# Kernel tuning notes

Measured on AMD Instinct MI355X. Metric: run time of the kernel, lower is better.

## Reference

```python
import jax, jax.numpy as jnp
import numpy as np

D = 384      # d_model
H = 6        # num_heads
K = 8        # k_neighbors
B = 8        # batch
N = 2048     # num points
EPS = 1e-5


def _layer_norm(x, g, b):
    m = jnp.mean(x, axis=-1, keepdims=True)
    v = jnp.var(x, axis=-1, keepdims=True)
    return (x - m) * jax.lax.rsqrt(v + EPS) * g + b


def setup_inputs() -> dict:
    key = jax.random.key(0)
    ks = jax.random.split(key, 12)
    s = 0.02
    return {
        "coords": jax.random.normal(ks[0], (B, 3, N), jnp.float32),
        "features": jax.random.normal(ks[1], (B, D, N), jnp.float32),
        "ln1_g": jnp.ones((D,), jnp.float32),
        "ln1_b": jnp.zeros((D,), jnp.float32),
        "w_qkv": jax.random.normal(ks[2], (D, 3 * D), jnp.float32) * s,
        "w_attn_out": jax.random.normal(ks[3], (D, D), jnp.float32) * s,
        "b_attn_out": jnp.zeros((D,), jnp.float32),
        "ga_wq": jax.random.normal(ks[4], (D, D), jnp.float32) * s,
        "ga_wk": jax.random.normal(ks[5], (D, D), jnp.float32) * s,
        "ga_wv": jax.random.normal(ks[6], (D, D), jnp.float32) * s,
        "merge_w": jax.random.normal(ks[7], (2 * D, D), jnp.float32) * s,
        "merge_b": jnp.zeros((D,), jnp.float32),
        "ln2_g": jnp.ones((D,), jnp.float32),
        "ln2_b": jnp.zeros((D,), jnp.float32),
        "ff_w1": jax.random.normal(ks[8], (D, 2 * D), jnp.float32) * s,
        "ff_b1": jnp.zeros((2 * D,), jnp.float32),
        "ff_w2": jax.random.normal(ks[9], (2 * D, D), jnp.float32) * s,
        "ff_b2": jnp.zeros((D,), jnp.float32),
    }


def reference(coords, features, ln1_g, ln1_b, w_qkv, w_attn_out, b_attn_out,
              ga_wq, ga_wk, ga_wv, merge_w, merge_b, ln2_g, ln2_b,
              ff_w1, ff_b1, ff_w2, ff_b2):
    b, d, n = features.shape
    dh = d // H
    f = jnp.swapaxes(features, 1, 2)          # [B, N, D]
    nf = _layer_norm(f, ln1_g, ln1_b)         # [B, N, D]

    # --- dense multi-head self-attention branch ---
    qkv = nf @ w_qkv                           # [B, N, 3D]
    q, k, v = jnp.split(qkv, 3, axis=-1)
    def heads(x):
        return x.reshape(b, n, H, dh).transpose(0, 2, 1, 3)  # [B, H, N, dh]
    scores = jnp.einsum('bhqd,bhkd->bhqk', heads(q), heads(k)) / jnp.sqrt(jnp.float32(dh))
    attn = jnp.einsum('bhqk,bhkd->bhqd', jax.nn.softmax(scores, axis=-1), heads(v))
    attn = attn.transpose(0, 2, 1, 3).reshape(b, n, d)
    attn = attn @ w_attn_out + b_attn_out      # output projection

    # --- KNN graph-attention branch over normalized features ---
    c = jnp.swapaxes(coords, 1, 2)             # [B, N, 3]
    sq = jnp.sum(c * c, axis=-1)               # [B, N]
    d2 = sq[:, :, None] + sq[:, None, :] - 2.0 * jnp.einsum('bnd,bmd->bnm', c, c)
    _, idx = jax.lax.top_k(-d2, K)             # [B, N, K] nearest-neighbor indices
    nbrs = jax.vmap(lambda fe, i: fe[i])(nf, idx)  # [B, N, K, D]
    gq = nf @ ga_wq                             # [B, N, D]
    gk = nbrs @ ga_wk                           # [B, N, K, D]
    gv = nbrs @ ga_wv
    gs = jnp.einsum('bnd,bnkd->bnk', gq, gk) / jnp.sqrt(jnp.float32(d))
    geom = jnp.einsum('bnk,bnkd->bnd', jax.nn.softmax(gs, axis=-1), gv)  # [B, N, D]

    # --- merge + residual + FFN ---
    merged = jnp.concatenate([attn, geom], axis=-1) @ merge_w + merge_b
    f = f + merged
    h = _layer_norm(f, ln2_g, ln2_b)
    f = f + (jax.nn.gelu(h @ ff_w1 + ff_b1) @ ff_w2 + ff_b2)
    return jnp.swapaxes(f, 1, 2)               # [B, D, N]
```

## Files before the change

### kernel.cpp

```cpp
#include <hip/hip_runtime.h>
#include <hip/hip_bf16.h>
#include <cstdint>

#define D_MODEL 384
#define NHEAD 6
#define DHEAD 64
#define NPTS 2048
#define BATCH 8

typedef __attribute__((ext_vector_type(8))) short short8;
typedef __attribute__((ext_vector_type(4))) short short4v;
typedef __attribute__((ext_vector_type(4))) float floatx4;
typedef __attribute__((ext_vector_type(2))) unsigned int u32x2;

__device__ __forceinline__ float bf2f(unsigned short u) {
    return __uint_as_float(((unsigned int)u) << 16);
}

__device__ __forceinline__ unsigned short f2bf(float f) {
    unsigned int u = __float_as_uint(f);
    unsigned int r = (u + 0x7FFFu + ((u >> 16) & 1u)) >> 16;
    return (unsigned short)r;
}

__device__ __forceinline__ unsigned cvtpk(float lo, float hi) {
    unsigned r;
    asm("v_cvt_pk_bf16_f32 %0, %1, %2" : "=v"(r) : "v"(lo), "v"(hi));
    return r;
}

__device__ __forceinline__ floatx4 mfma16(short4v a, short4v b, floatx4 c) {
#if __has_builtin(__builtin_amdgcn_mfma_f32_16x16x16bf16_1k)
    return __builtin_amdgcn_mfma_f32_16x16x16bf16_1k(a, b, c, 0, 0, 0);
#else
    floatx4 d;
    asm("v_mfma_f32_16x16x16_bf16 %0, %1, %2, %3" : "=v"(d) : "v"(a), "v"(b), "v"(c));
    return d;
#endif
}

__device__ __forceinline__ float gelu_tanh(float x) {
    float x3 = x * x * x;
    return 0.5f * x * (1.0f + tanhf(0.7978845608028654f * (x + 0.044715f * x3)));
}

__device__ __forceinline__ void gload_lds16(const unsigned short* g, unsigned short* l) {
    __builtin_amdgcn_global_load_lds(
        (const __attribute__((address_space(1))) unsigned int*)g,
        (__attribute__((address_space(3))) unsigned int*)l, 16, 0, 0);
}

__global__ __launch_bounds__(256) void k_wprep(
    const float* __restrict__ wqkv, const float* __restrict__ wao,
    const float* __restrict__ wq, const float* __restrict__ wk,
    const float* __restrict__ wv, const float* __restrict__ wm,
    const float* __restrict__ w1, const float* __restrict__ w2,
    unsigned short* __restrict__ qkvT, unsigned short* __restrict__ aoT,
    unsigned short* __restrict__ gaT, unsigned short* __restrict__ mT,
    unsigned short* __restrict__ f1T, unsigned short* __restrict__ f2T) {
    __shared__ float tile[32][33];
    int id = blockIdx.x;
    const float* src;
    unsigned short* dst;
    int K, N;
    if (id < 432)       {            src = wqkv; dst = qkvT;            K = 384; N = 1152; }
    else if (id < 576)  { id -= 432; src = wao;  dst = aoT;             K = 384; N = 384; }
    else if (id < 720)  { id -= 576; src = wq;   dst = gaT;             K = 384; N = 384; }
    else if (id < 864)  { id -= 720; src = wk;   dst = gaT + 384 * 384; K = 384; N = 384; }
    else if (id < 1008) { id -= 864; src = wv;   dst = gaT + 768 * 384; K = 384; N = 384; }
    else if (id < 1296) { id -= 1008; src = wm;  dst = mT;              K = 768; N = 384; }
    else if (id < 1584) { id -= 1296; src = w1;  dst = f1T;             K = 384; N = 768; }
    else                { id -= 1584; src = w2;  dst = f2T;             K = 768; N = 384; }
    int ntiles = N >> 5;
    int nt = id % ntiles, kt = id / ntiles;
    int tx = threadIdx.x, ty = threadIdx.y;
#pragma unroll
    for (int i = 0; i < 32; i += 8)
        tile[ty + i][tx] = src[(size_t)(kt * 32 + ty + i) * N + nt * 32 + tx];
    __syncthreads();
#pragma unroll
    for (int i = 0; i < 32; i += 8)
        dst[(size_t)(nt * 32 + ty + i) * K + kt * 32 + tx] = f2bf(tile[tx][ty + i]);
}

__global__ __launch_bounds__(256) void k_transpose_in(const float* __restrict__ feat,
                                                      unsigned short* __restrict__ f) {
    __shared__ float tile[32][33];
    int b = blockIdx.z;
    int n0 = blockIdx.x * 32, d0 = blockIdx.y * 32;
    int tx = threadIdx.x, ty = threadIdx.y;
#pragma unroll
    for (int i = 0; i < 32; i += 8)
        tile[ty + i][tx] = feat[((size_t)b * D_MODEL + d0 + ty + i) * NPTS + n0 + tx];
    __syncthreads();
#pragma unroll
    for (int i = 0; i < 32; i += 8)
        f[((size_t)b * NPTS + n0 + ty + i) * D_MODEL + d0 + tx] = f2bf(tile[tx][ty + i]);
}

__global__ __launch_bounds__(256) void k_transpose_out(const unsigned short* __restrict__ f,
                                                       float* __restrict__ out) {
    __shared__ float tile[32][33];
    int b = blockIdx.z;
    int d0 = blockIdx.x * 32, n0 = blockIdx.y * 32;
    int tx = threadIdx.x, ty = threadIdx.y;
#pragma unroll
    for (int i = 0; i < 32; i += 8)
        tile[ty + i][tx] = bf2f(f[((size_t)b * NPTS + n0 + ty + i) * D_MODEL + d0 + tx]);
    __syncthreads();
#pragma unroll
    for (int i = 0; i < 32; i += 8)
        out[((size_t)b * D_MODEL + d0 + ty + i) * NPTS + n0 + tx] = tile[tx][ty + i];
}

__global__ __launch_bounds__(256) void k_vt(const unsigned short* __restrict__ qkv,
                                            unsigned short* __restrict__ vt) {
    __shared__ unsigned short tile[32][33];
    int b = blockIdx.z;
    int h = blockIdx.y >> 1, d0 = (blockIdx.y & 1) * 32;
    int n0 = blockIdx.x * 32;
    int tx = threadIdx.x, ty = threadIdx.y;
#pragma unroll
    for (int i = 0; i < 32; i += 8)
        tile[ty + i][tx] =
            qkv[((size_t)b * NPTS + n0 + ty + i) * 1152 + 768 + h * 64 + d0 + tx];
    __syncthreads();
#pragma unroll
    for (int i = 0; i < 32; i += 8)
        vt[(((size_t)(b * NHEAD + h) * 64) + d0 + ty + i) * NPTS + n0 + tx] = tile[tx][ty + i];
}

__global__ __launch_bounds__(128) void k_layernorm(const unsigned short* __restrict__ x,
                                                   const float* __restrict__ g,
                                                   const float* __restrict__ bt,
                                                   unsigned short* __restrict__ y) {
    int row = blockIdx.x, t = threadIdx.x;
    const unsigned short* xr = x + (size_t)row * D_MODEL;
    float v0 = bf2f(xr[t]), v1 = bf2f(xr[t + 128]), v2 = bf2f(xr[t + 256]);
    float s = v0 + v1 + v2;
    float s2 = v0 * v0 + v1 * v1 + v2 * v2;
#pragma unroll
    for (int off = 32; off > 0; off >>= 1) {
        s += __shfl_xor(s, off, 64);
        s2 += __shfl_xor(s2, off, 64);
    }
    __shared__ float ps[2], ps2[2];
    if ((t & 63) == 0) { ps[t >> 6] = s; ps2[t >> 6] = s2; }
    __syncthreads();
    s = ps[0] + ps[1];
    s2 = ps2[0] + ps2[1];
    float mean = s * (1.0f / 384.0f);
    float var = s2 * (1.0f / 384.0f) - mean * mean;
    var = fmaxf(var, 0.0f);
    float inv = 1.0f / sqrtf(var + 1e-5f);
    unsigned short* yr = y + (size_t)row * D_MODEL;
    yr[t]       = f2bf((v0 - mean) * inv * g[t]       + bt[t]);
    yr[t + 128] = f2bf((v1 - mean) * inv * g[t + 128] + bt[t + 128]);
    yr[t + 256] = f2bf((v2 - mean) * inv * g[t + 256] + bt[t + 256]);
}

__global__ __launch_bounds__(256) void k_knn(const float* __restrict__ coords,
                                             int* __restrict__ idx) {
    __shared__ float4 cpts[NPTS];
    int b = blockIdx.x >> 9;
    int q0 = (blockIdx.x & 511) * 4;
    const float* cb = coords + (size_t)b * 3 * NPTS;
    int tid = threadIdx.x;
#pragma unroll
    for (int i = 0; i < 8; i++) {
        int m = tid + i * 256;
        float x = cb[m], y = cb[NPTS + m], z = cb[2 * NPTS + m];
        float sq = __fadd_rn(__fadd_rn(__fmul_rn(x, x), __fmul_rn(y, y)), __fmul_rn(z, z));
        cpts[m] = make_float4(x, y, z, sq);
    }
    __syncthreads();
    int wv = tid >> 6, lane = tid & 63;
    int n = q0 + wv;
    float4 qp = cpts[n];
    float qx = qp.x, qy = qp.y, qz = qp.z, sqn = qp.w;
    unsigned keys[32];
    unsigned h[8];
#pragma unroll
    for (int k = 0; k < 8; k++) h[k] = 0xFFFFFFFFu;
#pragma unroll
    for (int j = 0; j < 32; j++) {
        float4 cp = cpts[j * 64 + lane];
        float dot = __fadd_rn(__fadd_rn(__fmul_rn(qx, cp.x), __fmul_rn(qy, cp.y)),
                              __fmul_rn(qz, cp.z));
        float d2 = __fsub_rn(__fadd_rn(sqn, cp.w), __fmul_rn(2.0f, dot));
        unsigned u = __float_as_uint(d2);
        u ^= (unsigned)(((int)u >> 31)) | 0x80000000u;
        keys[j] = u;
        unsigned cur = u;
#pragma unroll
        for (int t2 = 0; t2 < 8; t2++) {
            unsigned lo = h[t2] < cur ? h[t2] : cur;
            cur = h[t2] < cur ? cur : h[t2];
            h[t2] = lo;
        }
    }
    unsigned curh = h[0];
    unsigned T8 = 0;
#pragma unroll
    for (int r = 0; r < 8; r++) {
        unsigned w = curh;
#pragma unroll
        for (int off = 1; off < 64; off <<= 1) {
            unsigned o = __shfl_xor(w, off, 64);
            w = o < w ? o : w;
        }
        T8 = w;
        if (r < 7) {
            unsigned long long mask = __ballot(curh == w);
            if (curh == w && (mask & ((1ull << lane) - 1ull)) == 0) {
#pragma unroll
                for (int t2 = 0; t2 < 7; t2++) h[t2] = h[t2 + 1];
                h[7] = 0xFFFFFFFFu;
                curh = h[0];
            }
        }
    }
    int* outr = idx + ((size_t)b * NPTS + n) * 8;
    int cnt = 0;
    unsigned meq = 0xFFFFFFFFu;
#pragma unroll
    for (int j = 0; j < 32; j++) {
        unsigned m = (unsigned)(j * 64 + lane);
        bool strict = keys[j] < T8;
        unsigned long long msk = __ballot(strict);
        if (strict) {
            int pos = cnt + (int)__popcll(msk & ((1ull << lane) - 1ull));
            outr[pos] = (int)m;
        }
        cnt += (int)__popcll(msk);
        if (keys[j] == T8 && m < meq) meq = m;
    }
    while (cnt < 8) {
        unsigned w = meq;
#pragma unroll
        for (int off = 1; off < 64; off <<= 1) {
            unsigned o = __shfl_xor(w, off, 64);
            w = o < w ? o : w;
        }
        bool winner = (meq == w);
        if (winner) outr[cnt] = (int)w;
        cnt++;
        if (cnt >= 8) break;
        if (winner) {
            meq = 0xFFFFFFFFu;
#pragma unroll
            for (int j = 0; j < 32; j++) {
                unsigned m = (unsigned)(j * 64 + lane);
                if (keys[j] == T8 && m > w && m < meq) meq = m;
            }
        }
    }
}

__global__ __launch_bounds__(256) void k_gemm(const unsigned short* __restrict__ A, int lda,
                                              const unsigned short* __restrict__ WT,
                                              const float* __restrict__ bias,
                                              const unsigned short* __restrict__ res,
                                              unsigned short* __restrict__ C, int ldc,
                                              int K, int act, int NX) {
    __shared__ unsigned short Alds[2 * 128 * 32];
    __shared__ unsigned short Wlds[2 * 128 * 32];
    int tid = threadIdx.x;
    int wv = tid >> 6, lane = tid & 63;
    int l15 = lane & 15, quad = lane >> 4;
    int id = blockIdx.x;
    int xcd = id & 7, slot = id >> 3;
    int y = xcd * 16 + slot / NX;
    int x = slot % NX;
    int row0 = y * 128, col0 = x * 128;
    int wm = wv >> 1, wn = wv & 1;
    int wbase = tid & 192;
    floatx4 acc[4][4];
#pragma unroll
    for (int i = 0; i < 4; i++)
#pragma unroll
        for (int j = 0; j < 4; j++) acc[i][j] = (floatx4){0.f, 0.f, 0.f, 0.f};
    for (int k0 = 0; k0 < K; k0 += 64) {
#pragma unroll
        for (int i = 0; i < 4; i++) {
            int idx = i * 256 + tid;
            int kc = idx >> 9, row = (idx >> 2) & 127, ko = idx & 3;
            unsigned short* ldst = Alds + (size_t)(i * 256 + wbase) * 8;
            gload_lds16(A + (size_t)(row0 + row) * lda + k0 + kc * 32 + ko * 8, ldst);
            unsigned short* ldstw = Wlds + (size_t)(i * 256 + wbase) * 8;
            gload_lds16(WT + (size_t)(col0 + row) * K + k0 + kc * 32 + ko * 8, ldstw);
        }
        __syncthreads();
#pragma unroll
        for (int kc = 0; kc < 2; kc++) {
            short8 af[4], bf[4];
#pragma unroll
            for (int i = 0; i < 4; i++)
                af[i] = *(const short8*)&Alds[kc * 4096 + (wm * 64 + i * 16 + l15) * 32 + quad * 8];
#pragma unroll
            for (int j = 0; j < 4; j++)
                bf[j] = *(const short8*)&Wlds[kc * 4096 + (wn * 64 + j * 16 + l15) * 32 + quad * 8];
#pragma unroll
            for (int i = 0; i < 4; i++)
#pragma unroll
                for (int j = 0; j < 4; j++)
                    acc[i][j] =
                        __builtin_amdgcn_mfma_f32_16x16x32_bf16(bf[j], af[i], acc[i][j], 0, 0, 0);
        }
        __syncthreads();
    }
#pragma unroll
    for (int i = 0; i < 4; i++) {
        int r = row0 + wm * 64 + i * 16 + l15;
#pragma unroll
        for (int j = 0; j < 4; j++) {
            int cb = col0 + wn * 64 + j * 16 + quad * 4;
            float4 bv = bias ? *(const float4*)(bias + cb) : make_float4(0.f, 0.f, 0.f, 0.f);
            float v0 = acc[i][j][0] + bv.x;
            float v1 = acc[i][j][1] + bv.y;
            float v2 = acc[i][j][2] + bv.z;
            float v3 = acc[i][j][3] + bv.w;
            if (act == 1) {
                v0 = gelu_tanh(v0); v1 = gelu_tanh(v1);
                v2 = gelu_tanh(v2); v3 = gelu_tanh(v3);
            }
            if (res) {
                uint2 rv = *(const uint2*)(res + (size_t)r * ldc + cb);
                const unsigned short* rs = (const unsigned short*)&rv;
                v0 += bf2f(rs[0]); v1 += bf2f(rs[1]);
                v2 += bf2f(rs[2]); v3 += bf2f(rs[3]);
            }
            ushort4 u;
            u.x = f2bf(v0); u.y = f2bf(v1); u.z = f2bf(v2); u.w = f2bf(v3);
            *(ushort4*)(C + (size_t)r * ldc + cb) = u;
        }
    }
}

__global__ __launch_bounds__(256, 3) void k_attn(const unsigned short* __restrict__ qkv,
                                                 const unsigned short* __restrict__ vt,
                                                 unsigned short* __restrict__ attn) {
    __shared__ unsigned short Klds[2][64 * 64];
    __shared__ unsigned short VTl[2][64 * 64];
    int id = blockIdx.x;
    int xcd = id & 7, slot = id >> 3;
    int pair = xcd * 6 + (slot >> 4);
    int tile = slot & 15;
    int b = pair / 6, h = pair % 6;
    int tid = threadIdx.x;
    int wv = tid >> 6, lane = tid & 63;
    int l15 = lane & 15, quad = lane >> 4;
    int qbase = tile * 128 + wv * 32;
    const unsigned short* qkvb = qkv + (size_t)b * NPTS * 1152;
    const unsigned short* vtb = vt + (size_t)(b * NHEAD + h) * 64 * NPTS;
    const float SC = 0.18033688011112042f;
    short8 qf[2][2];
#pragma unroll
    for (int qt = 0; qt < 2; qt++) {
        const unsigned short* qptr =
            qkvb + (size_t)(qbase + qt * 16 + l15) * 1152 + h * 64 + quad * 8;
        qf[qt][0] = *(const short8*)qptr;
        qf[qt][1] = *(const short8*)(qptr + 32);
#pragma unroll
        for (int g = 0; g < 2; g++) {
            short8 v = qf[qt][g];
#pragma unroll
            for (int e = 0; e < 8; e++)
                v[e] = (short)f2bf(bf2f((unsigned short)v[e]) * SC);
            qf[qt][g] = v;
        }
    }
    short4v ones4;
#pragma unroll
    for (int e = 0; e < 4; e++) ones4[e] = (short)0x3F80;
    int x7 = l15 & 7;
    int sk0 = ((quad ^ x7) << 4);
    int sk1 = (((quad + 4) ^ x7) << 4);
    int vslot[4];
#pragma unroll
    for (int kt = 0; kt < 4; kt++) vslot[kt] = (((kt * 2 + (quad >> 1)) ^ x7) << 4);
    int vsub = (quad & 1) * 8;
    int sdg = tid & 7;
    floatx4 o[2][4];
#pragma unroll
    for (int qt = 0; qt < 2; qt++)
#pragma unroll
        for (int ct = 0; ct < 4; ct++) o[qt][ct] = (floatx4){0.f, 0.f, 0.f, 0.f};
    floatx4 l4[2];
    l4[0] = (floatx4){0.f, 0.f, 0.f, 0.f};
    l4[1] = (floatx4){0.f, 0.f, 0.f, 0.f};

    auto stage = [&](int c, int k0) {
#pragma unroll
        for (int i = 0; i < 2; i++) {
            int sid = i * 256 + tid;
            int row = sid >> 3;
            int sl = sdg ^ (row & 7);
            gload_lds16(qkvb + (size_t)(k0 + row) * 1152 + 384 + h * 64 + sl * 8,
                        &Klds[c][(size_t)(i * 256 + (tid & 192)) * 8]);
            gload_lds16(vtb + (size_t)row * NPTS + k0 + sl * 8,
                        &VTl[c][(size_t)(i * 256 + (tid & 192)) * 8]);
        }
    };

    stage(0, 0);
    __syncthreads();
    for (int t = 0; t < 32; ++t) {
        int c = t & 1;
        if (t < 31) stage(c ^ 1, (t + 1) * 64);
        const char* Kb = (const char*)&Klds[c][0];
        const char* Vb = (const char*)&VTl[c][0];
        short8 kf[4][2];
#pragma unroll
        for (int ct = 0; ct < 4; ct++) {
            kf[ct][0] = *(const short8*)(Kb + (ct * 16 + l15) * 128 + sk0);
            kf[ct][1] = *(const short8*)(Kb + (ct * 16 + l15) * 128 + sk1);
        }
        short4v pf16[2][4];
#pragma unroll
        for (int qt = 0; qt < 2; qt++) {
#pragma unroll
            for (int ct = 0; ct < 4; ct++) {
                floatx4 z = (floatx4){0.f, 0.f, 0.f, 0.f};
                z = __builtin_amdgcn_mfma_f32_16x16x32_bf16(kf[ct][0], qf[qt][0], z, 0, 0, 0);
                z = __builtin_amdgcn_mfma_f32_16x16x32_bf16(kf[ct][1], qf[qt][1], z, 0, 0, 0);
                float p0 = __builtin_amdgcn_exp2f(z[0]);
                float p1 = __builtin_amdgcn_exp2f(z[1]);
                float p2 = __builtin_amdgcn_exp2f(z[2]);
                float p3 = __builtin_amdgcn_exp2f(z[3]);
                u32x2 pk;
                pk.x = cvtpk(p0, p1);
                pk.y = cvtpk(p2, p3);
                pf16[qt][ct] = __builtin_bit_cast(short4v, pk);
            }
        }
        const char* vb0 = Vb + l15 * 128 + vsub;
#pragma unroll
        for (int ctd = 0; ctd < 4; ctd++) {
            short4v va[4];
#pragma unroll
            for (int kt = 0; kt < 4; kt++)
                va[kt] = *(const short4v*)(vb0 + ctd * 2048 + vslot[kt]);
#pragma unroll
            for (int kt = 0; kt < 4; kt++) {
#pragma unroll
                for (int qt = 0; qt < 2; qt++)
                    o[qt][ctd] = mfma16(va[kt], pf16[qt][kt], o[qt][ctd]);
            }
        }
#pragma unroll
        for (int qt = 0; qt < 2; qt++)
#pragma unroll
            for (int kt = 0; kt < 4; kt++) l4[qt] = mfma16(ones4, pf16[qt][kt], l4[qt]);
        if (t < 31) __syncthreads();
    }
#pragma unroll
    for (int qt = 0; qt < 2; qt++) {
        float linv = 1.0f / l4[qt][0];
#pragma unroll
        for (int ct = 0; ct < 4; ct++) {
            ushort4 u;
            u.x = f2bf(o[qt][ct][0] * linv);
            u.y = f2bf(o[qt][ct][1] * linv);
            u.z = f2bf(o[qt][ct][2] * linv);
            u.w = f2bf(o[qt][ct][3] * linv);
            *(ushort4*)(attn + ((size_t)b * NPTS + qbase + qt * 16 + l15) * 384 + h * 64 +
                        ct * 16 + quad * 4) = u;
        }
    }
}

__global__ __launch_bounds__(64) void k_geom(const unsigned short* __restrict__ gap,
                                             const int* __restrict__ idx,
                                             unsigned short* __restrict__ cat) {
    int r = blockIdx.x;
    int b = r >> 11;
    int t = threadIdx.x;
    int nb[8];
#pragma unroll
    for (int k = 0; k < 8; k++) nb[k] = idx[(size_t)r * 8 + k];
    const unsigned short* gqr = gap + (size_t)r * 1152;
    float qv[6];
#pragma unroll
    for (int j = 0; j < 6; j++) qv[j] = bf2f(gqr[t + 64 * j]);
    float s[8];
#pragma unroll
    for (int k = 0; k < 8; k++) {
        const unsigned short* nkr = gap + ((size_t)b * NPTS + nb[k]) * 1152 + 384;
        float acc = 0.0f;
#pragma unroll
        for (int j = 0; j < 6; j++) acc += qv[j] * bf2f(nkr[t + 64 * j]);
#pragma unroll
        for (int mm = 32; mm > 0; mm >>= 1) acc += __shfl_xor(acc, mm, 64);
        s[k] = acc * 0.05103103630798287f;
    }
    float mx = s[0];
#pragma unroll
    for (int k = 1; k < 8; k++) mx = fmaxf(mx, s[k]);
    float w[8];
    float sum = 0.0f;
#pragma unroll
    for (int k = 0; k < 8; k++) { w[k] = __expf(s[k] - mx); sum += w[k]; }
    float inv = 1.0f / sum;
    unsigned short* outr = cat + (size_t)r * 768 + 384;
#pragma unroll
    for (int j = 0; j < 6; j++) {
        int d = t + 64 * j;
        float acc = 0.0f;
#pragma unroll
        for (int k = 0; k < 8; k++)
            acc += w[k] * bf2f(gap[((size_t)b * NPTS + nb[k]) * 1152 + 768 + d]);
        outr[d] = f2bf(acc * inv);
    }
}

extern "C" void kernel_launch(void* const* d_in, const int* in_sizes, int n_in,
                              void* d_out, int out_size, void* d_ws, size_t ws_size,
                              hipStream_t stream) {
    (void)in_sizes; (void)n_in; (void)out_size; (void)ws_size;
    const float* coords     = (const float*)d_in[0];
    const float* features   = (const float*)d_in[1];
    const float* ln1_g      = (const float*)d_in[2];
    const float* ln1_b      = (const float*)d_in[3];
    const float* w_qkv      = (const float*)d_in[4];
    const float* w_attn_out = (const float*)d_in[5];
    const float* b_attn_out = (const float*)d_in[6];
    const float* ga_wq      = (const float*)d_in[7];
    const float* ga_wk      = (const float*)d_in[8];
    const float* ga_wv      = (const float*)d_in[9];
    const float* merge_w    = (const float*)d_in[10];
    const float* merge_b    = (const float*)d_in[11];
    const float* ln2_g      = (const float*)d_in[12];
    const float* ln2_b      = (const float*)d_in[13];
    const float* ff_w1      = (const float*)d_in[14];
    const float* ff_b1      = (const float*)d_in[15];
    const float* ff_w2      = (const float*)d_in[16];
    const float* ff_b2      = (const float*)d_in[17];

    unsigned short* W0 = (unsigned short*)d_ws;
    const size_t SZ = (size_t)BATCH * NPTS * D_MODEL;
    unsigned short* F    = W0 + 0 * SZ;
    unsigned short* NF   = W0 + 1 * SZ;
    unsigned short* QKV  = W0 + 2 * SZ;
    unsigned short* ATTN = W0 + 5 * SZ;
    unsigned short* VT   = W0 + 6 * SZ;
    unsigned short* CAT  = W0 + 2 * SZ;
    unsigned short* GAP  = W0 + 4 * SZ;
    unsigned short* F2   = W0 + 4 * SZ;
    unsigned short* HB   = W0 + 1 * SZ;
    unsigned short* T1   = W0 + 5 * SZ;
    unsigned short* FFIN = W0 + 2 * SZ;
    int*            IDX  = (int*)(W0 + 7 * SZ);
    unsigned short* WTS  = W0 + 7 * SZ + 262144;
    unsigned short* qkvT = WTS;
    unsigned short* aoT  = qkvT + 442368;
    unsigned short* gaT  = aoT + 147456;
    unsigned short* mT   = gaT + 442368;
    unsigned short* f1T  = mT + 294912;
    unsigned short* f2T  = f1T + 294912;

    const int M = BATCH * NPTS;

    k_wprep<<<1872, dim3(32, 8), 0, stream>>>(w_qkv, w_attn_out, ga_wq, ga_wk, ga_wv,
                                              merge_w, ff_w1, ff_w2,
                                              qkvT, aoT, gaT, mT, f1T, f2T);
    k_transpose_in<<<dim3(NPTS / 32, D_MODEL / 32, BATCH), dim3(32, 8), 0, stream>>>(features, F);
    k_layernorm<<<M, 128, 0, stream>>>(F, ln1_g, ln1_b, NF);
    k_knn<<<BATCH * (NPTS / 4), 256, 0, stream>>>(coords, IDX);
    k_gemm<<<9 * 128, 256, 0, stream>>>(NF, 384, qkvT, nullptr, nullptr,
                                        QKV, 1152, 384, 0, 9);
    k_vt<<<dim3(NPTS / 32, 2 * NHEAD, BATCH), dim3(32, 8), 0, stream>>>(QKV, VT);
    k_attn<<<768, 256, 0, stream>>>(QKV, VT, ATTN);
    k_gemm<<<3 * 128, 256, 0, stream>>>(ATTN, 384, aoT, b_attn_out, nullptr,
                                        CAT, 768, 384, 0, 3);
    k_gemm<<<9 * 128, 256, 0, stream>>>(NF, 384, gaT, nullptr, nullptr,
                                        GAP, 1152, 384, 0, 9);
    k_geom<<<M, 64, 0, stream>>>(GAP, IDX, CAT);
    k_gemm<<<3 * 128, 256, 0, stream>>>(CAT, 768, mT, merge_b, F,
                                        F2, 384, 768, 0, 3);
    k_layernorm<<<M, 128, 0, stream>>>(F2, ln2_g, ln2_b, HB);
    k_gemm<<<6 * 128, 256, 0, stream>>>(HB, 384, f1T, ff_b1, nullptr,
                                        T1, 768, 384, 1, 6);
    k_gemm<<<3 * 128, 256, 0, stream>>>(T1, 768, f2T, ff_b2, F2,
                                        FFIN, 384, 768, 0, 3);
    k_transpose_out<<<dim3(D_MODEL / 32, NPTS / 32, BATCH), dim3(32, 8), 0, stream>>>(
        FFIN, (float*)d_out);
}
```

Before: 416.6 us.

## Software-pipeline attention loop: overlap QK softmax of tile t with PV of t-1

Restructures the attention main loop so the QK^T+exp chain for tile t is issued alongside the PV accumulation for tile t-1, using ping-pong probability registers and a 4-deep V LDS ring. The goal is to interleave the independent MFMA chains and hide exp and LDS latency behind matrix work. In exchange it raises register pressure (two P buffers) and LDS use (V buffers double), which can reduce occupancy under the 3-blocks-per-CU launch bound.

```diff
diff --git a/kernel.cpp b/kernel.cpp
--- a/kernel.cpp
+++ b/kernel.cpp
@@ -341,7 +341,7 @@
                                                  const unsigned short* __restrict__ vt,
                                                  unsigned short* __restrict__ attn) {
     __shared__ unsigned short Klds[2][64 * 64];
-    __shared__ unsigned short VTl[2][64 * 64];
+    __shared__ unsigned short VTl[4][64 * 64];
     int id = blockIdx.x;
     int xcd = id & 7, slot = id >> 3;
     int pair = xcd * 6 + (slot >> 4);
@@ -390,33 +390,27 @@
     l4[0] = (floatx4){0.f, 0.f, 0.f, 0.f};
     l4[1] = (floatx4){0.f, 0.f, 0.f, 0.f};
 
-    auto stage = [&](int c, int k0) {
+    auto stage = [&](int t) {
+        int k0 = t * 64;
 #pragma unroll
         for (int i = 0; i < 2; i++) {
             int sid = i * 256 + tid;
             int row = sid >> 3;
             int sl = sdg ^ (row & 7);
             gload_lds16(qkvb + (size_t)(k0 + row) * 1152 + 384 + h * 64 + sl * 8,
-                        &Klds[c][(size_t)(i * 256 + (tid & 192)) * 8]);
+                        &Klds[t & 1][(size_t)(i * 256 + (tid & 192)) * 8]);
             gload_lds16(vtb + (size_t)row * NPTS + k0 + sl * 8,
-                        &VTl[c][(size_t)(i * 256 + (tid & 192)) * 8]);
+                        &VTl[t & 3][(size_t)(i * 256 + (tid & 192)) * 8]);
         }
     };
-
-    stage(0, 0);
-    __syncthreads();
-    for (int t = 0; t < 32; ++t) {
-        int c = t & 1;
-        if (t < 31) stage(c ^ 1, (t + 1) * 64);
-        const char* Kb = (const char*)&Klds[c][0];
-        const char* Vb = (const char*)&VTl[c][0];
+    auto qkchain = [&](int t, short4v (&pfc)[2][4]) {
+        const char* Kb = (const char*)&Klds[t & 1][0];
         short8 kf[4][2];
 #pragma unroll
         for (int ct = 0; ct < 4; ct++) {
             kf[ct][0] = *(const short8*)(Kb + (ct * 16 + l15) * 128 + sk0);
             kf[ct][1] = *(const short8*)(Kb + (ct * 16 + l15) * 128 + sk1);
         }
-        short4v pf16[2][4];
 #pragma unroll
         for (int qt = 0; qt < 2; qt++) {
 #pragma unroll
@@ -431,29 +425,51 @@
                 u32x2 pk;
                 pk.x = cvtpk(p0, p1);
                 pk.y = cvtpk(p2, p3);
-                pf16[qt][ct] = __builtin_bit_cast(short4v, pk);
+                pfc[qt][ct] = __builtin_bit_cast(short4v, pk);
             }
         }
-        const char* vb0 = Vb + l15 * 128 + vsub;
+    };
+    auto pv = [&](int t, short4v (&pfp)[2][4]) {
+        const char* Vb = (const char*)&VTl[t & 3][0] + l15 * 128 + vsub;
 #pragma unroll
         for (int ctd = 0; ctd < 4; ctd++) {
             short4v va[4];
 #pragma unroll
             for (int kt = 0; kt < 4; kt++)
-                va[kt] = *(const short4v*)(vb0 + ctd * 2048 + vslot[kt]);
-#pragma unroll
-            for (int kt = 0; kt < 4; kt++) {
+                va[kt] = *(const short4v*)(Vb + ctd * 2048 + vslot[kt]);
+#pragma unroll
+            for (int kt = 0; kt < 4; kt++)
 #pragma unroll
                 for (int qt = 0; qt < 2; qt++)
-                    o[qt][ctd] = mfma16(va[kt], pf16[qt][kt], o[qt][ctd]);
-            }
+                    o[qt][ctd] = mfma16(va[kt], pfp[qt][kt], o[qt][ctd]);
         }
 #pragma unroll
         for (int qt = 0; qt < 2; qt++)
 #pragma unroll
-            for (int kt = 0; kt < 4; kt++) l4[qt] = mfma16(ones4, pf16[qt][kt], l4[qt]);
-        if (t < 31) __syncthreads();
-    }
+            for (int kt = 0; kt < 4; kt++) l4[qt] = mfma16(ones4, pfp[qt][kt], l4[qt]);
+    };
+
+    short4v pfA[2][4], pfB[2][4];
+    stage(0);
+    __syncthreads();
+    stage(1);
+    qkchain(0, pfA);
+    __syncthreads();
+    for (int tt = 0; tt < 15; ++tt) {
+        int t1 = 2 * tt + 1, t2 = 2 * tt + 2;
+        stage(t1 + 1);
+        qkchain(t1, pfB);
+        pv(t1 - 1, pfA);
+        __syncthreads();
+        stage(t2 + 1);
+        qkchain(t2, pfA);
+        pv(t2 - 1, pfB);
+        __syncthreads();
+    }
+    qkchain(31, pfB);
+    pv(30, pfA);
+    pv(31, pfB);
+
 #pragma unroll
     for (int qt = 0; qt < 2; qt++) {
         float linv = 1.0f / l4[qt][0];
```

Result: slower. 431.2 us (+3.5%).
